# Optimization experiments

Measured on AMD Instinct MI355X. Metric: run time of the kernel, lower is better.

The kernel has to match this reference:

```python
import jax, jax.numpy as jnp
import numpy as np

# --- stochastic-computing constants (match FSUMGUCell defaults) ---
BW_W = 8                      # FSULinearPC weight bitstream bitwidth
BW_M = 4                      # FSUMul bitwidth (shift-register depth)
DEPTH = 10                    # FSUAdd accumulator depth
ACC_MAX = 2.0 ** (DEPTH - 2)  # +256
ACC_MIN = -ACC_MAX
NW = 2 ** BW_W
NM = 2 ** BW_M
# deterministic pseudo-random comparison sequences (stand-in for UnarySim Sobol RNG)
_RNG_W = jnp.asarray(np.random.RandomState(0).permutation(NW), dtype=jnp.float32)
_RNG_WI = jnp.asarray(np.random.RandomState(1).permutation(NW), dtype=jnp.float32)
_RNG_M = jnp.asarray(np.random.RandomState(2).permutation(NM), dtype=jnp.float32)


def _fsu_add(acc, s, offset, scale):
    # FSUAdd (bipolar): accumulate (parallel count - offset), clamp, emit bit when acc >= scale
    acc = jnp.clip(acc + s - offset, ACC_MIN, ACC_MAX)
    out = (acc >= scale).astype(jnp.float32)
    return acc - out * scale, out


def _linear_pc(x_aug, w_src, t):
    # FSULinearPC (bipolar): weight bits generated by rate coding (source > rng[t]),
    # XNOR with input bits, summed into a parallel count. x_aug: [B, F+1] (bias col of 1s).
    wb_p = (w_src > _RNG_W[t % NW]).astype(jnp.float32)   # [O, F+1]
    wb_i = (w_src > _RNG_WI[t % NW]).astype(jnp.float32)
    return x_aug @ wb_p.T + (1.0 - x_aug) @ (1.0 - wb_i).T


def _fsu_mul(state, in0, in1):
    # FSUMul non-static bipolar: estimate P(in1) with a BW_M-bit shift register,
    # regenerate a bit via rng comparison; XNOR-style pos/inv paths gated by in0,
    # with conditionally-advanced rng indices (enable-signal semantics).
    sr, idx_p, idx_i = state
    sr = jnp.concatenate([sr[1:], in1[None]], axis=0)      # shift in newest bit
    cnt = sr.sum(0) * (NM / BW_M)                          # scale count to rng range
    bit_p = (cnt > _RNG_M[idx_p % NM]).astype(jnp.float32)
    bit_i = (cnt > _RNG_M[idx_i % NM]).astype(jnp.float32)
    out = in0 * bit_p + (1.0 - in0) * (1.0 - bit_i)        # disjoint paths -> OR == +
    idx_p = idx_p + in0.astype(jnp.int32)
    idx_i = idx_i + (1 - in0.astype(jnp.int32))
    return (sr, idx_p, idx_i), out


def _w_src(w, b):
    # SourceGen bipolar: binary value in [-1,1] -> integer source in [0, 2^BW_W]
    aug = jnp.concatenate([w, b[:, None]], axis=1)
    return jnp.round((jnp.clip(aug, -1.0, 1.0) + 1.0) * 0.5 * NW)


def _forward(x_bits, hx0, weight_ih, bias_ih, weight_hh, bias_hh):
    T, B, I = x_bits.shape
    H = hx0.shape[1]
    src_ih = _w_src(weight_ih, bias_ih)   # [2H, I+1]
    src_hh = _w_src(weight_hh, bias_hh)   # [2H, H+1]
    ones_col = jnp.ones((B, 1), jnp.float32)
    acc0 = jnp.zeros((B, H), jnp.float32)
    sr0 = jnp.tile((jnp.arange(BW_M) % 2).astype(jnp.float32)[:, None, None], (1, B, H))
    mul0 = (sr0, jnp.zeros((B, H), jnp.int32), jnp.zeros((B, H), jnp.int32))
    off_fg = (I + H + 2 - 1) / 2.0        # entry=I+H+2, scaled=False -> scale=1

    def step(carry, xt):
        h, a1, a2, a3, a4, a5, a6, m1, m2, m3, t = carry
        gate_i = _linear_pc(jnp.concatenate([xt, ones_col], 1), src_ih, t)  # [B, 2H]
        gate_h = _linear_pc(jnp.concatenate([h, ones_col], 1), src_hh, t)
        i_f, i_n = gate_i[:, :H], gate_i[:, H:]
        h_f, h_n = gate_h[:, :H], gate_h[:, H:]
        a1, fg_in = _fsu_add(a1, i_f + h_f, off_fg, 1.0)
        a2, fg = _fsu_add(a2, fg_in + 1.0, 0.0, 2.0)          # scaled (x+1)/2 hardsigmoid
        a3, h_n_bit = _fsu_add(a3, h_n, H / 2.0, 1.0)          # entry=H+1
        m1, ng_prod = _fsu_mul(m1, fg, h_n_bit)
        a4, i_n_bit = _fsu_add(a4, i_n, I / 2.0, 1.0)          # entry=I+1
        a5, ng = _fsu_add(a5, i_n_bit + ng_prod, 0.5, 1.0)     # entry=2
        m2, fgi_prod = _fsu_mul(m2, 1.0 - fg, ng)
        m3, fg_prod = _fsu_mul(m3, fg, h)
        a6, hy = _fsu_add(a6, ng + fgi_prod + fg_prod, 1.0, 1.0)  # entry=3
        return (hy, a1, a2, a3, a4, a5, a6, m1, m2, m3, t + 1), hy

    carry0 = (hx0, acc0, acc0, acc0, acc0, acc0, acc0, mul0, mul0, mul0, jnp.int32(0))
    _, hy_stream = jax.lax.scan(step, carry0, x_bits)
    return hy_stream  # [T, B, H] unary bitstream of hidden state


def setup_inputs():
    key = jax.random.key(0)
    ks = jax.random.split(key, 6)
    T, B, I, H = 64, 128, 1024, 1024
    x_bits = jax.random.bernoulli(ks[0], 0.5, (T, B, I)).astype(jnp.float32)
    hx0 = jax.random.bernoulli(ks[1], 0.5, (B, H)).astype(jnp.float32)
    weight_ih = jax.random.uniform(ks[2], (2 * H, I), jnp.float32, -1.0, 1.0)
    bias_ih = jax.random.uniform(ks[3], (2 * H,), jnp.float32, -1.0, 1.0)
    weight_hh = jax.random.uniform(ks[4], (2 * H, H), jnp.float32, -1.0, 1.0)
    bias_hh = jax.random.uniform(ks[5], (2 * H,), jnp.float32, -1.0, 1.0)
    return {"x_bits": x_bits, "hx0": hx0, "weight_ih": weight_ih, "bias_ih": bias_ih,
            "weight_hh": weight_hh, "bias_hh": bias_hh}


def reference(x_bits, hx0, weight_ih, bias_ih, weight_hh, bias_hh):
    return _forward(x_bits, hx0, weight_ih, bias_ih, weight_hh, bias_hh)
```

## Files before the change

kernel.cpp:

```cpp
#include <hip/hip_runtime.h>


#define NBLK 256
#define NTHR 512

#define WS_BAR_SUB   0u
#define WS_BAR_MST   1024u
#define WS_BAR_FLG   2048u
#define WS_HDONE  4096u
#define WS_RNGW   8192u
#define WS_RNGWI  9216u
#define WS_RNGM   10240u
#define WS_SRCB   12288u
#define WS_SRCW   20480u
#define WS_XP     8409088u
#define WS_HW     9457664u
#define WS_DT     9490432u
#define WS_MASKS  10539008u

struct SRng {
  unsigned mt[3][624];
  unsigned yb[3][624];
  unsigned draws[3][1248];
  int perm[3][256];
};
struct SC {
  unsigned short rows[16][1028];
  int rngw[64];
  int rngwi[64];
};
struct SL {
  unsigned long long mask2[64*34];
  unsigned xb[32*34];
  unsigned hb[32*34];
  unsigned hraw[64*17];
  int dl[64];
  int rngm[16];
};
union SU { SRng r; SC c; SL l; };

__device__ __forceinline__ unsigned mt_temper(unsigned y){
  y ^= y >> 11;
  y ^= (y << 7)  & 0x9d2c5680u;
  y ^= (y << 15) & 0xefc60000u;
  y ^= y >> 18;
  return y;
}

__device__ void mt_regen_serial(unsigned* mt){
  for (int i = 0; i < 624; i++){
    unsigned y = (mt[i] & 0x80000000u) | (mt[(i+1)%624] & 0x7fffffffu);
    mt[i] = mt[(i+397)%624] ^ (y >> 1) ^ ((y & 1u) ? 0x9908b0dfu : 0u);
  }
}

__device__ __forceinline__ unsigned long long llc_load64(const unsigned* p){
  unsigned long long v;
  asm volatile("global_load_dwordx2 %0, %1, off sc0 sc1\n\t"
               "s_waitcnt vmcnt(0)"
               : "=&v"(v) : "v"(p) : "memory");
  return v;
}

__device__ void rng_gen(SU* sm, int* rngw, int* rngwi, int* rngm){
  const int tid = threadIdx.x;
  const int wv = tid >> 6, lane = tid & 63;
  const bool act = (wv < 3);
  if (act && lane == 0){
    unsigned* mt = sm->r.mt[wv];
    mt[0] = (unsigned)wv;
    for (int i = 1; i < 624; i++)
      mt[i] = 1812433253u * (mt[i-1] ^ (mt[i-1] >> 30)) + (unsigned)i;
  }
  __syncthreads();
  for (int r = 0; r < 2; r++){
    if (act){
      unsigned* mt = sm->r.mt[wv]; unsigned* yb = sm->r.yb[wv];
      for (int i = lane; i < 623; i += 64)
        yb[i] = (mt[i] & 0x80000000u) | (mt[i+1] & 0x7fffffffu);
    }
    __syncthreads();
    if (act){
      unsigned* mt = sm->r.mt[wv]; unsigned* yb = sm->r.yb[wv];
      for (int i = lane; i < 227; i += 64){
        unsigned y = yb[i];
        mt[i] = mt[i+397] ^ (y >> 1) ^ ((y & 1u) ? 0x9908b0dfu : 0u);
      }
    }
    __syncthreads();
    if (act){
      unsigned* mt = sm->r.mt[wv]; unsigned* yb = sm->r.yb[wv];
      for (int i = 227 + lane; i < 454; i += 64){
        unsigned y = yb[i];
        mt[i] = mt[i-227] ^ (y >> 1) ^ ((y & 1u) ? 0x9908b0dfu : 0u);
      }
    }
    __syncthreads();
    if (act){
      unsigned* mt = sm->r.mt[wv]; unsigned* yb = sm->r.yb[wv];
      for (int i = 454 + lane; i < 624; i += 64){
        unsigned y = (i < 623) ? yb[i]
                   : ((mt[623] & 0x80000000u) | (mt[0] & 0x7fffffffu));
        mt[i] = mt[i-227] ^ (y >> 1) ^ ((y & 1u) ? 0x9908b0dfu : 0u);
      }
    }
    __syncthreads();
    if (act){
      unsigned* mt = sm->r.mt[wv];
      for (int i = lane; i < 624; i += 64)
        sm->r.draws[wv][r*624 + i] = mt_temper(mt[i]);
    }
    __syncthreads();
  }
  if (act && lane == 0){
    const int n = (wv == 2) ? 16 : 256;
    int* perm = sm->r.perm[wv];
    for (int i = 0; i < n; i++) perm[i] = i;
    int dp = 0, spos = 624;
    unsigned* mt = sm->r.mt[wv];
    for (int i = n - 1; i > 0; i--){
      unsigned mask = (unsigned)i;
      mask |= mask >> 1; mask |= mask >> 2; mask |= mask >> 4;
      mask |= mask >> 8; mask |= mask >> 16;
      unsigned v;
      do {
        unsigned d;
        if (dp < 1248) d = sm->r.draws[wv][dp++];
        else {
          if (spos >= 624){ mt_regen_serial(mt); spos = 0; }
          d = mt_temper(mt[spos++]);
        }
        v = d & mask;
      } while (v > (unsigned)i);
      int tmp = perm[i]; perm[i] = perm[v]; perm[v] = tmp;
    }
    int* dst = (wv == 0) ? rngw : (wv == 1) ? rngwi : rngm;
    for (int i = 0; i < n; i++) dst[i] = perm[i];
  }
}

__device__ __forceinline__ void gbar_full(unsigned char* ws, unsigned ep){
  __syncthreads();
  if (threadIdx.x == 0){
    __threadfence();
    unsigned* sub = (unsigned*)(ws + WS_BAR_SUB + (blockIdx.x & 7)*128);
    unsigned old = atomicAdd(sub, 1u);
    if (old == ep*32u - 1u){
      unsigned* mst = (unsigned*)(ws + WS_BAR_MST);
      unsigned mo = atomicAdd(mst, 1u);
      if (mo == ep*8u - 1u){
        for (int i = 0; i < 8; i++)
          __hip_atomic_store((unsigned*)(ws + WS_BAR_FLG + i*128), ep,
                             __ATOMIC_RELAXED, __HIP_MEMORY_SCOPE_AGENT);
      }
    }
    const unsigned* fl = (const unsigned*)(ws + WS_BAR_FLG + (blockIdx.x & 7)*128);
    while (__hip_atomic_load(fl, __ATOMIC_RELAXED, __HIP_MEMORY_SCOPE_AGENT) < ep)
      __builtin_amdgcn_s_sleep(8);
  }
  __syncthreads();
  __threadfence();
}

__device__ __forceinline__ int clampi(int v){
  v = v < -512 ? -512 : v;
  v = v >  512 ?  512 : v;
  return v;
}

__global__ void __launch_bounds__(NTHR)
fsu_kernel(const float* __restrict__ x, const float* __restrict__ hx0,
           const float* __restrict__ wih, const float* __restrict__ bih,
           const float* __restrict__ whh, const float* __restrict__ bhh,
           float* __restrict__ out, unsigned char* __restrict__ ws)
{
  __shared__ SU sm;
  const int tid = threadIdx.x;
  const int bid = blockIdx.x;

  int* rngw  = (int*)(ws + WS_RNGW);
  int* rngwi = (int*)(ws + WS_RNGWI);
  int* rngm  = (int*)(ws + WS_RNGM);
  unsigned short* srcb = (unsigned short*)(ws + WS_SRCB);
  unsigned short* srcw = (unsigned short*)(ws + WS_SRCW);
  unsigned* xp   = (unsigned*)(ws + WS_XP);
  unsigned* hw   = (unsigned*)(ws + WS_HW);
  unsigned* hdone = (unsigned*)(ws + WS_HDONE);
  int* Dt = (int*)(ws + WS_DT);
  unsigned long long* masks = (unsigned long long*)(ws + WS_MASKS);

  if (bid == 0){
    rng_gen(&sm, rngw, rngwi, rngm);
  } else {
    const int gtid = (bid - 1)*NTHR + tid;
    const int lane = tid & 63;
    const int gw = gtid >> 6;
    const int nw = (NBLK-1)*(NTHR/64);
    const int nthr = (NBLK-1)*NTHR;
    for (int ch = gw; ch < 131072; ch += nw){
      float v = x[(size_t)ch*64 + lane];
      unsigned long long bal = __ballot(v != 0.0f);
      if ((lane & 31) == 0) xp[ch*2 + (lane >> 5)] = (unsigned)(bal >> lane);
    }
    for (int idx = gtid; idx < 4096; idx += nthr){
      int bg2 = idx >> 10, jt2 = (idx >> 4) & 63, rp2 = idx & 15;
      int r0 = bg2*32 + 2*rp2;
      unsigned v = 0;
      for (int j = 0; j < 16; j++){
        v |= (hx0[(size_t)r0*1024 + jt2*16 + j] != 0.0f) ? (1u<<j) : 0u;
        v |= (hx0[(size_t)(r0+1)*1024 + jt2*16 + j] != 0.0f) ? (1u<<(16+j)) : 0u;
      }
      hw[idx] = v;
    }
    for (int idx = gtid; idx < 4096*1024; idx += nthr){
      int c = idx >> 10, k = idx & 1023;
      float wv2 = (c < 2048) ? wih[(size_t)c*1024 + k] : whh[(size_t)(c - 2048)*1024 + k];
      float cl = fminf(fmaxf(wv2, -1.0f), 1.0f);
      srcw[idx] = (unsigned short)(int)rintf((cl + 1.0f)*0.5f*256.0f);
    }
    for (int c = gtid; c < 4096; c += nthr){
      float bv = (c < 2048) ? bih[c] : bhh[c - 2048];
      float cl = fminf(fmaxf(bv, -1.0f), 1.0f);
      srcb[c] = (unsigned short)(int)rintf((cl + 1.0f)*0.5f*256.0f);
    }
  }
  gbar_full(ws, 1u);

  {
    const int c0 = bid * 16;
    const unsigned* srcw32 = (const unsigned*)srcw;
    for (int q = tid; q < 16*512; q += NTHR){
      int r = q >> 9, w = q & 511;
      ((unsigned*)&sm.c.rows[r][0])[w] = srcw32[(size_t)(c0 + r)*512 + w];
    }
    if (tid < 64) sm.c.rngw[tid] = rngw[tid];
    if (tid >= 64 && tid < 128) sm.c.rngwi[tid - 64] = rngwi[tid - 64];
    __syncthreads();
    for (int rr = 0; rr < 2; rr++){
      int row = tid + rr*NTHR;
      int t = row >> 4, lc = row & 15, col = c0 + lc;
      int rp = sm.c.rngw[t], ri = sm.c.rngwi[t];
      int hi = rp > ri ? rp : ri;
      int lo1 = (rp < ri ? rp : ri) + 1;
      bool rihi = (ri >= rp);
      const unsigned* srow = (const unsigned*)&sm.c.rows[lc][0];
      unsigned long long* gdst = masks + ((size_t)t*4096 + col)*32;
      int cnti = 0;
      for (int w = 0; w < 32; w++){
        unsigned pos = 0, neg = 0;
        #pragma unroll
        for (int i2 = 15; i2 >= 0; i2--){
          unsigned v2 = srow[w*16 + i2];
          int vH = (int)(v2 >> 16);
          int vL = (int)(v2 & 0xFFFFu);
          pos = (pos << 1) | ((unsigned)(hi - vH) >> 31);
          neg = (neg << 1) | ((unsigned)(vH - lo1) >> 31);
          pos = (pos << 1) | ((unsigned)(hi - vL) >> 31);
          neg = (neg << 1) | ((unsigned)(vL - lo1) >> 31);
        }
        gdst[w] = (unsigned long long)pos | ((unsigned long long)neg << 32);
        cnti += rihi ? __popc(pos) : (32 - __popc(neg));
      }
      Dt[t*4096 + col] = 1024 - cnti + (((int)srcb[col] > rp) ? 1 : 0);
    }
  }
  gbar_full(ws, 2u);

  const int jt = bid & 63, bg = bid >> 6;
  const int j0 = jt * 16, b0 = bg * 32;
  const int b_l = tid >> 4, j_l = tid & 15;
  const int bglob = b0 + b_l;

  int hcur = (hx0[(size_t)bglob*1024 + j0 + j_l] != 0.0f) ? 1 : 0;
  int A1=0,A2=0,A3=0,A4=0,A5=0,A6=0;
  unsigned sr1=10u, sr2=10u, sr3=10u;
  int i1p=0,i1i=0,i2p=0,i2i=0,i3p=0,i3i=0;

  if (tid < 16) sm.l.rngm[tid] = rngm[tid];

  const unsigned* msrc = (const unsigned*)masks;
  unsigned* mlds = (unsigned*)sm.l.mask2;

  {
    #pragma unroll
    for (int i = 0; i < 8; i++){
      int q = tid + i*NTHR;
      int r = q >> 6, qq = q & 63;
      int c = (r >> 4)*1024 + j0 + (r & 15);
      mlds[r*68 + qq] = msrc[((size_t)0*4096 + c)*64 + qq];
    }
    #pragma unroll
    for (int i = 0; i < 2; i++){
      int q = tid + i*NTHR;
      int bb = q >> 5, w = q & 31;
      sm.l.xb[bb*34 + w] = xp[((size_t)0*128 + b0 + bb)*32 + w];
    }
    {
      unsigned long long hv = llc_load64(&hw[bg*1024 + 2*tid]);
      int q0 = 2*tid, q1 = 2*tid + 1;
      sm.l.hraw[(q0 >> 4)*17 + (q0 & 15)] = (unsigned)hv;
      sm.l.hraw[(q1 >> 4)*17 + (q1 & 15)] = (unsigned)(hv >> 32);
    }
    if (tid < 64){
      int c = (tid >> 4)*1024 + j0 + (tid & 15);
      sm.l.dl[tid] = Dt[0*4096 + c];
    }
    __syncthreads();
    #pragma unroll
    for (int i = 0; i < 2; i++){
      int idx = tid + i*NTHR;
      int bb = idx >> 5, w = idx & 31;
      int rp = bb >> 1, sh = (bb & 1) << 4;
      unsigned lo = (sm.l.hraw[(2*w)*17 + rp] >> sh) & 0xFFFFu;
      unsigned hi = (sm.l.hraw[(2*w + 1)*17 + rp] >> sh) & 0xFFFFu;
      sm.l.hb[bb*34 + w] = lo | (hi << 16);
    }
    __syncthreads();
  }

  for (int t = 0; t < 64; t++){
    const int par = t & 1;

    int p0=0,n0=0,p1=0,n1=0,p2=0,n2=0,p3=0,n3=0;
    const ulonglong2* m0p = (const ulonglong2*)&sm.l.mask2[(0*16 + j_l)*34];
    const ulonglong2* m1p = (const ulonglong2*)&sm.l.mask2[(1*16 + j_l)*34];
    const ulonglong2* m2p = (const ulonglong2*)&sm.l.mask2[(2*16 + j_l)*34];
    const ulonglong2* m3p = (const ulonglong2*)&sm.l.mask2[(3*16 + j_l)*34];
    const uint2* xrow = (const uint2*)&sm.l.xb[b_l*34];
    const uint2* hrow = (const uint2*)&sm.l.hb[b_l*34];
    #pragma unroll
    for (int w2 = 0; w2 < 16; w2++){
      uint2 xv = xrow[w2], hv = hrow[w2];
      ulonglong2 a = m0p[w2];
      p0 += __popc(xv.x & (unsigned)a.x) + __popc(xv.y & (unsigned)a.y);
      n0 += __popc(xv.x & (unsigned)(a.x >> 32)) + __popc(xv.y & (unsigned)(a.y >> 32));
      ulonglong2 b = m1p[w2];
      p1 += __popc(xv.x & (unsigned)b.x) + __popc(xv.y & (unsigned)b.y);
      n1 += __popc(xv.x & (unsigned)(b.x >> 32)) + __popc(xv.y & (unsigned)(b.y >> 32));
      ulonglong2 c2 = m2p[w2];
      p2 += __popc(hv.x & (unsigned)c2.x) + __popc(hv.y & (unsigned)c2.y);
      n2 += __popc(hv.x & (unsigned)(c2.x >> 32)) + __popc(hv.y & (unsigned)(c2.y >> 32));
      ulonglong2 d = m3p[w2];
      p3 += __popc(hv.x & (unsigned)d.x) + __popc(hv.y & (unsigned)d.y);
      n3 += __popc(hv.x & (unsigned)(d.x >> 32)) + __popc(hv.y & (unsigned)(d.y >> 32));
    }
    const int g_if = sm.l.dl[0*16 + j_l] + p0 - n0;
    const int g_in = sm.l.dl[1*16 + j_l] + p1 - n1;
    const int g_hf = sm.l.dl[2*16 + j_l] + p2 - n2;
    const int g_hn = sm.l.dl[3*16 + j_l] + p3 - n3;

    int s1 = g_if + g_hf;
    A1 = clampi(A1 + 2*s1 - 2049);
    int fg_in = (A1 >= 2); A1 -= fg_in << 1;
    A2 = clampi(A2 + ((fg_in + 1) << 1));
    int fg = (A2 >= 4); A2 -= fg << 2;
    A3 = clampi(A3 + (g_hn << 1) - 1024);
    int hnb = (A3 >= 2); A3 -= hnb << 1;

    sr1 = ((sr1 >> 1) | ((unsigned)hnb << 3)) & 0xFu;
    int ng_prod;
    {
      int cv = __popc(sr1) << 2;
      int bp = cv > sm.l.rngm[i1p & 15];
      int bi = cv > sm.l.rngm[i1i & 15];
      ng_prod = fg ? bp : (1 - bi);
      i1p += fg; i1i += 1 - fg;
    }
    A4 = clampi(A4 + (g_in << 1) - 1024);
    int inb = (A4 >= 2); A4 -= inb << 1;
    A5 = clampi(A5 + ((inb + ng_prod) << 1) - 1);
    int ng = (A5 >= 2); A5 -= ng << 1;

    sr2 = ((sr2 >> 1) | ((unsigned)ng << 3)) & 0xFu;
    int fgi;
    {
      int cv = __popc(sr2) << 2;
      int bp = cv > sm.l.rngm[i2p & 15];
      int bi = cv > sm.l.rngm[i2i & 15];
      fgi = (1 - fg) ? bp : (1 - bi);
      i2p += 1 - fg; i2i += fg;
    }
    sr3 = ((sr3 >> 1) | ((unsigned)hcur << 3)) & 0xFu;
    int fgp;
    {
      int cv = __popc(sr3) << 2;
      int bp = cv > sm.l.rngm[i3p & 15];
      int bi = cv > sm.l.rngm[i3i & 15];
      fgp = fg ? bp : (1 - bi);
      i3p += fg; i3i += 1 - fg;
    }
    A6 = clampi(A6 + ((ng + fgi + fgp) << 1) - 2);
    int hy = (A6 >= 2); A6 -= hy << 1;

    out[(size_t)t*131072 + (size_t)bglob*1024 + j0 + j_l] = (float)hy;
    hcur = hy;

    if (t < 63){
      unsigned long long bal = __ballot(hy);
      if ((tid & 31) == 0){
        unsigned v = (unsigned)(bal >> (tid & 32));
        unsigned old = atomicExch(
            &hw[((par ^ 1)*4 + bg)*1024 + jt*16 + (tid >> 5)], v);
        asm volatile("" :: "v"(old));
      }
      __syncthreads();
      if (tid == 0){
        unsigned old2 = atomicExch(&hdone[bg*64 + jt], (unsigned)(t + 1));
        asm volatile("" :: "v"(old2));
      }

      unsigned mreg[8], xreg[2];
      int dreg = 0;
      #pragma unroll
      for (int i = 0; i < 8; i++){
        int q = tid + i*NTHR;
        int r = q >> 6, qq = q & 63;
        int c = (r >> 4)*1024 + j0 + (r & 15);
        mreg[i] = msrc[((size_t)(t+1)*4096 + c)*64 + qq];
      }
      #pragma unroll
      for (int i = 0; i < 2; i++){
        int q = tid + i*NTHR;
        int bb = q >> 5, w = q & 31;
        xreg[i] = xp[((size_t)(t+1)*128 + b0 + bb)*32 + w];
      }
      if (tid < 64){
        int c = (tid >> 4)*1024 + j0 + (tid & 15);
        dreg = Dt[(t+1)*4096 + c];
      }

      if (tid < 64){
        const unsigned ep = (unsigned)(t + 1);
        unsigned* slot = hdone + bg*64 + tid;
        while (true){
          unsigned v = __hip_atomic_load(slot, __ATOMIC_RELAXED,
                                         __HIP_MEMORY_SCOPE_AGENT);
          if (__all((int)(v >= ep))) break;
          __builtin_amdgcn_s_sleep(1);
        }
      }
      __syncthreads();

      {
        unsigned long long hv =
            llc_load64(&hw[((par ^ 1)*4 + bg)*1024 + 2*tid]);
        int q0 = 2*tid, q1 = 2*tid + 1;
        sm.l.hraw[(q0 >> 4)*17 + (q0 & 15)] = (unsigned)hv;
        sm.l.hraw[(q1 >> 4)*17 + (q1 & 15)] = (unsigned)(hv >> 32);
      }
      #pragma unroll
      for (int i = 0; i < 8; i++){
        int q = tid + i*NTHR;
        int r = q >> 6, qq = q & 63;
        mlds[r*68 + qq] = mreg[i];
      }
      #pragma unroll
      for (int i = 0; i < 2; i++){
        int q = tid + i*NTHR;
        int bb = q >> 5, w = q & 31;
        sm.l.xb[bb*34 + w] = xreg[i];
      }
      if (tid < 64) sm.l.dl[tid] = dreg;
      __syncthreads();

      #pragma unroll
      for (int i = 0; i < 2; i++){
        int idx = tid + i*NTHR;
        int bb = idx >> 5, w = idx & 31;
        int rp = bb >> 1, sh = (bb & 1) << 4;
        unsigned lo = (sm.l.hraw[(2*w)*17 + rp] >> sh) & 0xFFFFu;
        unsigned hi = (sm.l.hraw[(2*w + 1)*17 + rp] >> sh) & 0xFFFFu;
        sm.l.hb[bb*34 + w] = lo | (hi << 16);
      }
      __syncthreads();
    }
  }
}

extern "C" void kernel_launch(void* const* d_in, const int* in_sizes, int n_in,
                              void* d_out, int out_size, void* d_ws, size_t ws_size,
                              hipStream_t stream)
{
  (void)in_sizes; (void)n_in; (void)out_size; (void)ws_size;
  const float* x   = (const float*)d_in[0];
  const float* hx0 = (const float*)d_in[1];
  const float* wih = (const float*)d_in[2];
  const float* bih = (const float*)d_in[3];
  const float* whh = (const float*)d_in[4];
  const float* bhh = (const float*)d_in[5];
  float* out = (float*)d_out;
  unsigned char* ws = (unsigned char*)d_ws;

  hipMemsetAsync(d_ws, 0, 8192, stream);

  void* args[] = { (void*)&x, (void*)&hx0, (void*)&wih, (void*)&bih,
                   (void*)&whh, (void*)&bhh, (void*)&out, (void*)&ws };
  hipLaunchCooperativeKernel(reinterpret_cast<void*>(fsu_kernel),
                             dim3(NBLK), dim3(NTHR), args, 0, stream);
}
```

Measured before the change: 520.8 us.

## Tag hidden-state words with epoch to replace separate done flags

Each per-step hidden-state word becomes 64-bit, carrying the bit data plus a step epoch in the upper half. A single relaxed atomic store then both publishes the data and signals readiness, which removes the separate atomicExch on the hdone counter and the ordering it required. Readers poll the tagged words directly, so the data and flag handshake shares one memory location. The output store is moved after the publish, the workspace layout shifts, and memsets are adjusted to clear the new hw region. This doubles the bytes polled and exchanged per step and relies on relaxed 64-bit atomics being single-copy atomic.

Result: no change. 517.8 us (-0.6%).

```diff
diff --git a/kernel.cpp b/kernel.cpp
--- a/kernel.cpp
+++ b/kernel.cpp
@@ -7,7 +7,6 @@
 #define WS_BAR_SUB   0u
 #define WS_BAR_MST   1024u
 #define WS_BAR_FLG   2048u
-#define WS_HDONE  4096u
 #define WS_RNGW   8192u
 #define WS_RNGWI  9216u
 #define WS_RNGM   10240u
@@ -15,8 +14,8 @@
 #define WS_SRCW   20480u
 #define WS_XP     8409088u
 #define WS_HW     9457664u
-#define WS_DT     9490432u
-#define WS_MASKS  10539008u
+#define WS_DT     9523200u
+#define WS_MASKS  10571776u
 
 struct SRng {
   unsigned mt[3][624];
@@ -52,14 +51,6 @@
     unsigned y = (mt[i] & 0x80000000u) | (mt[(i+1)%624] & 0x7fffffffu);
     mt[i] = mt[(i+397)%624] ^ (y >> 1) ^ ((y & 1u) ? 0x9908b0dfu : 0u);
   }
-}
-
-__device__ __forceinline__ unsigned long long llc_load64(const unsigned* p){
-  unsigned long long v;
-  asm volatile("global_load_dwordx2 %0, %1, off sc0 sc1\n\t"
-               "s_waitcnt vmcnt(0)"
-               : "=&v"(v) : "v"(p) : "memory");
-  return v;
 }
 
 __device__ void rng_gen(SU* sm, int* rngw, int* rngwi, int* rngm){
@@ -184,8 +175,7 @@
   unsigned short* srcb = (unsigned short*)(ws + WS_SRCB);
   unsigned short* srcw = (unsigned short*)(ws + WS_SRCW);
   unsigned* xp   = (unsigned*)(ws + WS_XP);
-  unsigned* hw   = (unsigned*)(ws + WS_HW);
-  unsigned* hdone = (unsigned*)(ws + WS_HDONE);
+  unsigned long long* hw = (unsigned long long*)(ws + WS_HW);
   int* Dt = (int*)(ws + WS_DT);
   unsigned long long* masks = (unsigned long long*)(ws + WS_MASKS);
 
@@ -210,7 +200,7 @@
         v |= (hx0[(size_t)r0*1024 + jt2*16 + j] != 0.0f) ? (1u<<j) : 0u;
         v |= (hx0[(size_t)(r0+1)*1024 + jt2*16 + j] != 0.0f) ? (1u<<(16+j)) : 0u;
       }
-      hw[idx] = v;
+      hw[idx] = (unsigned long long)v;
     }
     for (int idx = gtid; idx < 4096*1024; idx += nthr){
       int c = idx >> 10, k = idx & 1023;
@@ -295,11 +285,13 @@
       int bb = q >> 5, w = q & 31;
       sm.l.xb[bb*34 + w] = xp[((size_t)0*128 + b0 + bb)*32 + w];
     }
-    {
-      unsigned long long hv = llc_load64(&hw[bg*1024 + 2*tid]);
-      int q0 = 2*tid, q1 = 2*tid + 1;
-      sm.l.hraw[(q0 >> 4)*17 + (q0 & 15)] = (unsigned)hv;
-      sm.l.hraw[(q1 >> 4)*17 + (q1 & 15)] = (unsigned)(hv >> 32);
+    #pragma unroll
+    for (int i = 0; i < 2; i++){
+      int q = tid + i*NTHR;
+      unsigned long long v = __hip_atomic_load(&hw[(size_t)bg*1024 + q],
+                                               __ATOMIC_RELAXED,
+                                               __HIP_MEMORY_SCOPE_AGENT);
+      sm.l.hraw[(q >> 4)*17 + (q & 15)] = (unsigned)v;
     }
     if (tid < 64){
       int c = (tid >> 4)*1024 + j0 + (tid & 15);
@@ -391,23 +383,23 @@
     }
     A6 = clampi(A6 + ((ng + fgi + fgp) << 1) - 2);
     int hy = (A6 >= 2); A6 -= hy << 1;
-
-    out[(size_t)t*131072 + (size_t)bglob*1024 + j0 + j_l] = (float)hy;
     hcur = hy;
 
     if (t < 63){
       unsigned long long bal = __ballot(hy);
       if ((tid & 31) == 0){
-        unsigned v = (unsigned)(bal >> (tid & 32));
-        unsigned old = atomicExch(
-            &hw[((par ^ 1)*4 + bg)*1024 + jt*16 + (tid >> 5)], v);
-        asm volatile("" :: "v"(old));
-      }
+        unsigned data = (unsigned)(bal >> (tid & 32));
+        unsigned long long val = (unsigned long long)data
+                               | ((unsigned long long)(unsigned)(t + 1) << 32);
+        __hip_atomic_store(
+            &hw[(((size_t)(par ^ 1)*4 + bg)*64 + jt)*16 + (tid >> 5)], val,
+            __ATOMIC_RELAXED, __HIP_MEMORY_SCOPE_AGENT);
+      }
+    }
+    out[(size_t)t*131072 + (size_t)bglob*1024 + j0 + j_l] = (float)hy;
+
+    if (t < 63){
       __syncthreads();
-      if (tid == 0){
-        unsigned old2 = atomicExch(&hdone[bg*64 + jt], (unsigned)(t + 1));
-        asm volatile("" :: "v"(old2));
-      }
 
       unsigned mreg[8], xreg[2];
       int dreg = 0;
@@ -429,24 +421,32 @@
         dreg = Dt[(t+1)*4096 + c];
       }
 
+      const unsigned ep = (unsigned)(t + 1);
       if (tid < 64){
-        const unsigned ep = (unsigned)(t + 1);
-        unsigned* slot = hdone + bg*64 + tid;
+        const unsigned long long* slot =
+            &hw[(((size_t)(par ^ 1)*4 + bg)*64 + tid)*16];
         while (true){
-          unsigned v = __hip_atomic_load(slot, __ATOMIC_RELAXED,
-                                         __HIP_MEMORY_SCOPE_AGENT);
-          if (__all((int)(v >= ep))) break;
+          unsigned long long v = __hip_atomic_load(slot, __ATOMIC_RELAXED,
+                                                   __HIP_MEMORY_SCOPE_AGENT);
+          if (__all((int)((unsigned)(v >> 32) >= ep))) break;
+          __builtin_amdgcn_s_sleep(2);
+        }
+      }
+      __syncthreads();
+
+      #pragma unroll
+      for (int i = 0; i < 2; i++){
+        int q = tid + i*NTHR;
+        const unsigned long long* slot =
+            &hw[((size_t)(par ^ 1)*4 + bg)*1024 + q];
+        unsigned long long v;
+        while (true){
+          v = __hip_atomic_load(slot, __ATOMIC_RELAXED,
+                                __HIP_MEMORY_SCOPE_AGENT);
+          if ((unsigned)(v >> 32) >= ep) break;
           __builtin_amdgcn_s_sleep(1);
         }
-      }
-      __syncthreads();
-
-      {
-        unsigned long long hv =
-            llc_load64(&hw[((par ^ 1)*4 + bg)*1024 + 2*tid]);
-        int q0 = 2*tid, q1 = 2*tid + 1;
-        sm.l.hraw[(q0 >> 4)*17 + (q0 & 15)] = (unsigned)hv;
-        sm.l.hraw[(q1 >> 4)*17 + (q1 & 15)] = (unsigned)(hv >> 32);
+        sm.l.hraw[(q >> 4)*17 + (q & 15)] = (unsigned)v;
       }
       #pragma unroll
       for (int i = 0; i < 8; i++){
@@ -491,7 +491,8 @@
   float* out = (float*)d_out;
   unsigned char* ws = (unsigned char*)d_ws;
 
-  hipMemsetAsync(d_ws, 0, 8192, stream);
+  hipMemsetAsync(d_ws, 0, 4096, stream);
+  hipMemsetAsync(ws + WS_HW, 0, 65536, stream);
 
   void* args[] = { (void*)&x, (void*)&hx0, (void*)&wih, (void*)&bih,
                    (void*)&whh, (void*)&bhh, (void*)&out, (void*)&ws };
```
